# Kernel tuning notes

Hardware: AMD Instinct MI355X
Metric: run time of the kernel (lower is better)

Reference implementation:

```python
import jax, jax.numpy as jnp
import numpy as np

N_QUBITS = 10
N_LAYERS = 4
BATCH = 4096


def _apply_1q_batched(state, gate, q):
    # state: [B, 2,2,...,2]; gate: [B, 2, 2] (per-sample angles)
    s = jnp.moveaxis(state, 1 + q, -1)
    s = jnp.einsum('b...i,bji->b...j', s, gate)
    return jnp.moveaxis(s, -1, 1 + q)


def _apply_1q(state, gate, q):
    # gate: [2, 2] shared across batch
    s = jnp.moveaxis(state, 1 + q, -1)
    s = jnp.einsum('b...i,ji->b...j', s, gate)
    return jnp.moveaxis(s, -1, 1 + q)


def _apply_cnot(state, c, t):
    # bring control axis to 1 and target axis to 2, flip target where control==1
    s = jnp.moveaxis(state, (1 + c, 1 + t), (1, 2))
    s = jnp.concatenate([s[:, :1], s[:, 1:, ::-1]], axis=1)
    return jnp.moveaxis(s, (1, 2), (1 + c, 1 + t))


def _ry_rz_gate(theta_y, theta_z):
    # RZ(theta_z) @ RY(theta_y), both scalars -> [2, 2] complex
    hy = theta_y * 0.5
    cy, sy = jnp.cos(hy), jnp.sin(hy)
    ry = jnp.stack([jnp.stack([cy, -sy]), jnp.stack([sy, cy])]).astype(jnp.complex64)
    hz = theta_z * 0.5
    ph = jnp.exp(1j * jnp.stack([-hz, hz]).astype(jnp.complex64))  # diag of RZ
    return ph[:, None] * ry


def setup_inputs() -> dict:
    key = jax.random.key(0)
    kx, kp = jax.random.split(key)
    x = jax.random.uniform(kx, (BATCH, N_QUBITS), dtype=jnp.float32,
                           minval=-np.pi, maxval=np.pi)
    params = 0.5 * jax.random.normal(kp, (N_LAYERS, 2 * N_QUBITS), dtype=jnp.float32)
    return {"x": x, "params": params}


def reference(x, params):
    B, n = x.shape
    L = params.shape[0]
    dim = 2 ** n
    # |0...0> for every sample
    state = jnp.zeros((B, dim), jnp.complex64).at[:, 0].set(1.0)
    state = state.reshape((B,) + (2,) * n)

    # data encoding: RY(x[b, q]) on qubit q, per-sample angles
    half = x * 0.5
    c, s = jnp.cos(half), jnp.sin(half)  # [B, n]
    for q in range(n):
        g = jnp.stack([jnp.stack([c[:, q], -s[:, q]], -1),
                       jnp.stack([s[:, q], c[:, q]], -1)], -2).astype(jnp.complex64)  # [B,2,2]
        state = _apply_1q_batched(state, g, q)

    # variational layers: RY then RZ (fused) per qubit, then CNOT ring
    for l in range(L):
        for q in range(n):
            state = _apply_1q(state, _ry_rz_gate(params[l, q], params[l, n + q]), q)
        for q in range(n):
            state = _apply_cnot(state, q, (q + 1) % n)

    # <Z_q> = sum over basis states of |amp|^2 * (+1 if bit_q==0 else -1)
    probs = jnp.abs(state.reshape(B, dim)) ** 2  # float32 [B, 2^n]
    idx = jnp.arange(dim)
    bits = (idx[None, :] >> (n - 1 - jnp.arange(n))[:, None]) & 1  # [n, 2^n]
    signs = (1.0 - 2.0 * bits).astype(probs.dtype)
    return jnp.einsum('bs,qs->bq', probs, signs)  # [B, n]
```

## Files before the change

kernel.cpp:

```cpp
#include <hip/hip_runtime.h>

#define NQ 10

#if __has_builtin(__builtin_amdgcn_permlane16_swap)
#define HAVE_PLSWAP 1
#endif

typedef float v2f __attribute__((ext_vector_type(2)));

template<int M>
__device__ __forceinline__ float lx(float v) {
    if constexpr (M == 1)
        return __int_as_float(__builtin_amdgcn_mov_dpp(__float_as_int(v), 0xB1, 0xF, 0xF, true));
    else if constexpr (M == 2)
        return __int_as_float(__builtin_amdgcn_mov_dpp(__float_as_int(v), 0x4E, 0xF, 0xF, true));
    else if constexpr (M == 4) {
        int t = __builtin_amdgcn_mov_dpp(__float_as_int(v), 0x141, 0xF, 0xF, true);
        return __int_as_float(__builtin_amdgcn_mov_dpp(t, 0x1B, 0xF, 0xF, true));
    } else if constexpr (M == 8)
        return __int_as_float(__builtin_amdgcn_mov_dpp(__float_as_int(v), 0x128, 0xF, 0xF, true));
    else if constexpr (M == 16)
        return __int_as_float(__builtin_amdgcn_ds_swizzle(__float_as_int(v), (16 << 10) | 0x1F));
    else
        return __shfl_xor(v, M, 64);
}

template<int M>
__device__ __forceinline__ v2f lx2(v2f v) {
    v2f r;
    r.x = lx<M>(v.x);
    r.y = lx<M>(v.y);
    return r;
}

template<int M>
__device__ __forceinline__ void xch(float& a, float& b) {
#ifdef HAVE_PLSWAP
    if constexpr (M == 16) {
        auto r1 = __builtin_amdgcn_permlane16_swap(__float_as_uint(a), __float_as_uint(b), false, false);
        auto r2 = __builtin_amdgcn_permlane16_swap(r1[1], r1[0], false, false);
        a = __uint_as_float(r2[0]);
        b = __uint_as_float(r2[1]);
    } else {
        auto r1 = __builtin_amdgcn_permlane32_swap(__float_as_uint(a), __float_as_uint(b), false, false);
        auto r2 = __builtin_amdgcn_permlane32_swap(r1[1], r1[0], false, false);
        a = __uint_as_float(r2[0]);
        b = __uint_as_float(r2[1]);
    }
#else
    a = lx<M>(a);
    b = lx<M>(b);
#endif
}

template<int M>
__device__ __forceinline__ void xch2(v2f& a, v2f& b) {
    float ax = a.x, bx = b.x, ay = a.y, by = b.y;
    xch<M>(ax, bx);
    xch<M>(ay, by);
    a.x = ax; a.y = ay; b.x = bx; b.y = by;
}

__device__ __forceinline__ v2f cmul(v2f a, v2f b) {
    v2f n; n.x = -a.y; n.y = a.y;
    return a.xx * b + n * b.yx;
}

__device__ __forceinline__ v2f bperm2(int addr, v2f v) {
    v2f r;
    r.x = __int_as_float(__builtin_amdgcn_ds_bpermute(addr, __float_as_int(v.x)));
    r.y = __int_as_float(__builtin_amdgcn_ds_bpermute(addr, __float_as_int(v.y)));
    return r;
}

template<int M>
__device__ __forceinline__ void ry_lane(v2f st[16], int lane, float c, float s) {
    const float cB = (lane & M) ? s : -s;
#pragma unroll
    for (int r = 0; r < 16; ++r) {
        v2f part = lx2<M>(st[r]);
        st[r] = c * st[r] + cB * part;
    }
}

template<int M>
__device__ __forceinline__ void ry_lane_x(v2f st[16], int lane, float c, float s) {
    const float cB = (lane & M) ? s : -s;
#pragma unroll
    for (int r = 0; r < 16; r += 2) {
        v2f pa = st[r], pb = st[r + 1];
        xch2<M>(pa, pb);
        st[r]     = c * st[r]     + cB * pa;
        st[r + 1] = c * st[r + 1] + cB * pb;
    }
}

template<int RB>
__device__ __forceinline__ void ry_reg(v2f st[16], float c, float s) {
#pragma unroll
    for (int r = 0; r < 16; ++r) {
        if (r & RB) continue;
        v2f a0 = st[r], a1 = st[r | RB];
        st[r]      = c * a0 - s * a1;
        st[r | RB] = s * a0 + c * a1;
    }
}

template<int MC, int RB>
__device__ __forceinline__ void cnot_lane_reg(v2f st[16], int lane) {
    const bool sel = (lane & MC) != 0;
#pragma unroll
    for (int r = 0; r < 16; ++r) {
        if (r & RB) continue;
        v2f lo = st[r], hi = st[r | RB];
        st[r]      = sel ? hi : lo;
        st[r | RB] = sel ? lo : hi;
    }
}

template<int RC, int RT>
__device__ __forceinline__ void cnot_reg_reg(v2f st[16]) {
#pragma unroll
    for (int r = 0; r < 16; ++r) {
        if ((r & RC) && !(r & RT)) {
            v2f t = st[r];
            st[r] = st[r | RT];
            st[r | RT] = t;
        }
    }
}

__device__ __forceinline__ void cnot_q9_q0(v2f st[16]) {
#pragma unroll
    for (int i = 0; i < 4; ++i) {
        const int ra = 4 * i + 1, rb = 4 * i + 3;
        xch2<32>(st[ra], st[rb]);
    }
}

__device__ __forceinline__ float wht64(float v, int lane) {
    float t;
    t = lx<1>(v);  v = (lane & 1)  ? (t - v) : (v + t);
    t = lx<2>(v);  v = (lane & 2)  ? (t - v) : (v + t);
    t = lx<4>(v);  v = (lane & 4)  ? (t - v) : (v + t);
    t = lx<8>(v);  v = (lane & 8)  ? (t - v) : (v + t);
    t = lx<16>(v); v = (lane & 16) ? (t - v) : (v + t);
    t = lx<32>(v); v = (lane & 32) ? (t - v) : (v + t);
    return v;
}

__global__ __launch_bounds__(256)
void pqc_kernel(const float* __restrict__ x,
                const float* __restrict__ params,
                float* __restrict__ out, int B) {
    const int lane = threadIdx.x & 63;
    const int wave = threadIdx.x >> 6;
    const int b = blockIdx.x * 4 + wave;
    if (b >= B) return;

    const float* xb = x + (long)b * NQ;
    const float* p0 = params;
    float a0,b0,a1,b1,a2,b2,a3,b3,a4,b4,a5,b5,a6,b6,a7,b7,a8,b8,a9,b9;
    float cz0,sz0,cz1,sz1,cz2,sz2,cz3,sz3,cz4,sz4,cz5,sz5,cz6,sz6,cz7,sz7,cz8,sz8,cz9,sz9;
    __sincosf(0.5f * (xb[0] + p0[0]), &b0, &a0);
    __sincosf(0.5f * (xb[1] + p0[1]), &b1, &a1);
    __sincosf(0.5f * (xb[2] + p0[2]), &b2, &a2);
    __sincosf(0.5f * (xb[3] + p0[3]), &b3, &a3);
    __sincosf(0.5f * (xb[4] + p0[4]), &b4, &a4);
    __sincosf(0.5f * (xb[5] + p0[5]), &b5, &a5);
    __sincosf(0.5f * (xb[6] + p0[6]), &b6, &a6);
    __sincosf(0.5f * (xb[7] + p0[7]), &b7, &a7);
    __sincosf(0.5f * (xb[8] + p0[8]), &b8, &a8);
    __sincosf(0.5f * (xb[9] + p0[9]), &b9, &a9);
    __sincosf(0.5f * p0[10], &sz0, &cz0);
    __sincosf(0.5f * p0[11], &sz1, &cz1);
    __sincosf(0.5f * p0[12], &sz2, &cz2);
    __sincosf(0.5f * p0[13], &sz3, &cz3);
    __sincosf(0.5f * p0[14], &sz4, &cz4);
    __sincosf(0.5f * p0[15], &sz5, &cz5);
    __sincosf(0.5f * p0[16], &sz6, &cz6);
    __sincosf(0.5f * p0[17], &sz7, &cz7);
    __sincosf(0.5f * p0[18], &sz8, &cz8);
    __sincosf(0.5f * p0[19], &sz9, &cz9);

    float R = ((lane & 32) ? b0 : a0) * ((lane & 16) ? b1 : a1)
            * ((lane & 8)  ? b2 : a2) * ((lane & 4)  ? b3 : a3)
            * ((lane & 2)  ? b4 : a4) * ((lane & 1)  ? b5 : a5);
    v2f P; P.x = cz0; P.y = (lane & 32) ? sz0 : -sz0;
    { v2f t; t.x = cz1; t.y = (lane & 16) ? sz1 : -sz1; P = cmul(P, t); }
    { v2f t; t.x = cz2; t.y = (lane & 8)  ? sz2 : -sz2; P = cmul(P, t); }
    { v2f t; t.x = cz3; t.y = (lane & 4)  ? sz3 : -sz3; P = cmul(P, t); }
    { v2f t; t.x = cz4; t.y = (lane & 2)  ? sz4 : -sz4; P = cmul(P, t); }
    { v2f t; t.x = cz5; t.y = (lane & 1)  ? sz5 : -sz5; P = cmul(P, t); }
    v2f laneC = R * P;

    v2f u6l = { a6 * cz6, -a6 * sz6 }, u6h = { b6 * cz6, b6 * sz6 };
    v2f u7l = { a7 * cz7, -a7 * sz7 }, u7h = { b7 * cz7, b7 * sz7 };
    v2f u8l = { a8 * cz8, -a8 * sz8 }, u8h = { b8 * cz8, b8 * sz8 };
    v2f u9l = { a9 * cz9, -a9 * sz9 }, u9h = { b9 * cz9, b9 * sz9 };
    v2f A2[4] = { cmul(u6l, u7l), cmul(u6l, u7h), cmul(u6h, u7l), cmul(u6h, u7h) };
    v2f B2[4] = { cmul(u8l, u9l), cmul(u8l, u9h), cmul(u8h, u9l), cmul(u8h, u9h) };
    v2f LA[4] = { cmul(laneC, A2[0]), cmul(laneC, A2[1]),
                  cmul(laneC, A2[2]), cmul(laneC, A2[3]) };

    v2f st[16];
#pragma unroll
    for (int r = 0; r < 16; ++r) st[r] = cmul(LA[r >> 2], B2[r & 3]);

    {
        const int addr = ((lane ^ (lane >> 1)) & 63) << 2;
#pragma unroll
        for (int r = 0; r < 16; ++r) st[r] = bperm2(addr, st[r]);
        cnot_lane_reg<1, 8>(st, lane);
        cnot_reg_reg<8, 4>(st);
        cnot_reg_reg<4, 2>(st);
        cnot_reg_reg<2, 1>(st);
        cnot_q9_q0(st);
    }

    float c, s;
#pragma unroll
    for (int l = 1; l < 4; ++l) {
        const float* pl = params + l * 2 * NQ;

        __sincosf(0.5f * pl[0], &s, &c); ry_lane_x<32>(st, lane, c, s);
        __sincosf(0.5f * pl[1], &s, &c); ry_lane_x<16>(st, lane, c, s);
        __sincosf(0.5f * pl[2], &s, &c); ry_lane<8>(st, lane, c, s);
        __sincosf(0.5f * pl[3], &s, &c); ry_lane<4>(st, lane, c, s);
        __sincosf(0.5f * pl[4], &s, &c); ry_lane<2>(st, lane, c, s);
        __sincosf(0.5f * pl[5], &s, &c); ry_lane<1>(st, lane, c, s);
        __sincosf(0.5f * pl[6], &s, &c); ry_reg<8>(st, c, s);
        __sincosf(0.5f * pl[7], &s, &c); ry_reg<4>(st, c, s);
        __sincosf(0.5f * pl[8], &s, &c); ry_reg<2>(st, c, s);
        __sincosf(0.5f * pl[9], &s, &c); ry_reg<1>(st, c, s);

        if (l < 3) {
            float sz, cz;
            __sincosf(0.5f * pl[10], &sz, &cz);
            v2f PL; PL.x = cz; PL.y = (lane & 32) ? sz : -sz;
            __sincosf(0.5f * pl[11], &sz, &cz);
            { v2f t; t.x = cz; t.y = (lane & 16) ? sz : -sz; PL = cmul(PL, t); }
            __sincosf(0.5f * pl[12], &sz, &cz);
            { v2f t; t.x = cz; t.y = (lane & 8)  ? sz : -sz; PL = cmul(PL, t); }
            __sincosf(0.5f * pl[13], &sz, &cz);
            { v2f t; t.x = cz; t.y = (lane & 4)  ? sz : -sz; PL = cmul(PL, t); }
            __sincosf(0.5f * pl[14], &sz, &cz);
            { v2f t; t.x = cz; t.y = (lane & 2)  ? sz : -sz; PL = cmul(PL, t); }
            __sincosf(0.5f * pl[15], &sz, &cz);
            { v2f t; t.x = cz; t.y = (lane & 1)  ? sz : -sz; PL = cmul(PL, t); }

            float z6s, z6c, z7s, z7c, z8s, z8c, z9s, z9c;
            __sincosf(0.5f * pl[16], &z6s, &z6c);
            __sincosf(0.5f * pl[17], &z7s, &z7c);
            __sincosf(0.5f * pl[18], &z8s, &z8c);
            __sincosf(0.5f * pl[19], &z9s, &z9c);
            v2f A[4], Bb[4];
#pragma unroll
            for (int k = 0; k < 4; ++k) {
                v2f t6; t6.x = z6c; t6.y = (k & 2) ? z6s : -z6s;
                v2f t7; t7.x = z7c; t7.y = (k & 1) ? z7s : -z7s;
                A[k] = cmul(cmul(t6, t7), PL);
                v2f t8; t8.x = z8c; t8.y = (k & 2) ? z8s : -z8s;
                v2f t9; t9.x = z9c; t9.y = (k & 1) ? z9s : -z9s;
                Bb[k] = cmul(t8, t9);
            }
#pragma unroll
            for (int r = 0; r < 16; ++r)
                st[r] = cmul(cmul(st[r], A[r >> 2]), Bb[r & 3]);

            const int addr = ((lane ^ (lane >> 1)) & 63) << 2;
#pragma unroll
            for (int r = 0; r < 16; ++r) st[r] = bperm2(addr, st[r]);
            cnot_lane_reg<1, 8>(st, lane);
            cnot_reg_reg<8, 4>(st);
            cnot_reg_reg<4, 2>(st);
            cnot_reg_reg<2, 1>(st);
            cnot_q9_q0(st);
        }
    }

    float lane_sum = 0.f, A3 = 0.f, A32 = 0.f, A321 = 0.f, A3210 = 0.f;
#pragma unroll
    for (int r = 0; r < 16; ++r) {
        float p = st[r].x * st[r].x + st[r].y * st[r].y;
        const int p3 = (r >> 3) & 1;
        const int p32 = p3 ^ ((r >> 2) & 1);
        const int p321 = p32 ^ ((r >> 1) & 1);
        const int p3210 = p321 ^ (r & 1);
        lane_sum += p;
        A3    += p3    ? -p : p;
        A32   += p32   ? -p : p;
        A321  += p321  ? -p : p;
        A3210 += p3210 ? -p : p;
    }
    const float wLS   = wht64(lane_sum, lane);
    const float w3    = wht64(A3, lane);
    const float w32   = wht64(A32, lane);
    const float w321  = wht64(A321, lane);
    const float w3210 = wht64(A3210, lane);

    const long base = (long)b * NQ;
    if (lane == 31) out[base + 0] = w3210;
    if (lane == 48) out[base + 1] = wLS;
    if (lane == 56) out[base + 2] = wLS;
    if (lane == 60) out[base + 3] = wLS;
    if (lane == 62) out[base + 4] = wLS;
    if (lane == 63) {
        out[base + 5] = wLS;
        out[base + 6] = w3;
        out[base + 7] = w32;
        out[base + 8] = w321;
        out[base + 9] = w3210;
    }
}

extern "C" void kernel_launch(void* const* d_in, const int* in_sizes, int n_in,
                              void* d_out, int out_size, void* d_ws, size_t ws_size,
                              hipStream_t stream) {
    const float* x = (const float*)d_in[0];
    const float* params = (const float*)d_in[1];
    float* out = (float*)d_out;
    const int B = in_sizes[0] / NQ;
    const int grid = (B + 3) / 4;
    pqc_kernel<<<grid, 256, 0, stream>>>(x, params, out, B);
}
```

Before: 78.83 us.

## Absorb CNOT rings into GF(2) basis change instead of permuting amplitudes

```diff
diff --git a/kernel.cpp b/kernel.cpp
--- a/kernel.cpp
+++ b/kernel.cpp
@@ -2,63 +2,90 @@
 
 #define NQ 10
 
-#if __has_builtin(__builtin_amdgcn_permlane16_swap)
-#define HAVE_PLSWAP 1
-#endif
-
 typedef float v2f __attribute__((ext_vector_type(2)));
 
+struct M10 { unsigned r[10]; };
+
+constexpr M10 mk_R() {
+    M10 A{};
+    A.r[0] = 0b1111111110u;
+    for (int k = 1; k < 10; ++k) A.r[k] = (1u << (k + 1)) - 1u;
+    return A;
+}
+constexpr M10 mk_Rinv() {
+    M10 A{};
+    A.r[0] = (1u << 0) | (1u << 9);
+    A.r[1] = (1u << 0) | (1u << 1) | (1u << 9);
+    for (int k = 2; k < 10; ++k) A.r[k] = (1u << (k - 1)) | (1u << k);
+    return A;
+}
+constexpr M10 mmul(M10 A, M10 B) {
+    M10 C{};
+    for (int k = 0; k < 10; ++k) {
+        unsigned v = 0;
+        for (int j = 0; j < 10; ++j)
+            if ((A.r[k] >> j) & 1u) v ^= B.r[j];
+        C.r[k] = v;
+    }
+    return C;
+}
+constexpr M10 RF  = mk_R();
+constexpr M10 RV  = mk_Rinv();
+constexpr M10 RF2 = mmul(RF, RF);
+constexpr M10 RF3 = mmul(RF2, RF);
+constexpr M10 RF4 = mmul(RF2, RF2);
+constexpr M10 RV2 = mmul(RV, RV);
+constexpr M10 RV3 = mmul(RV2, RV);
+
+constexpr bool isI(M10 A) {
+    for (int k = 0; k < 10; ++k) if (A.r[k] != (1u << k)) return false;
+    return true;
+}
+static_assert(isI(mmul(RF, RV)), "Rinv wrong");
+static_assert(isI(mmul(RV3, RF3)), "powers wrong");
+
+constexpr unsigned colq(M10 A, int q) {
+    unsigned m = 0;
+    for (int k = 0; k < 10; ++k) m |= ((A.r[k] >> q) & 1u) << k;
+    return m;
+}
+constexpr int laneM(unsigned qm) {
+    int m = 0;
+    for (int q = 0; q <= 5; ++q) if ((qm >> q) & 1u) m |= 1 << (5 - q);
+    return m;
+}
+constexpr int regM(unsigned qm) {
+    int m = 0;
+    for (int q = 6; q <= 9; ++q) if ((qm >> q) & 1u) m |= 1 << (9 - q);
+    return m;
+}
+
+template<int CTRL>
+__device__ __forceinline__ float dppmov(float v) {
+    return __int_as_float(__builtin_amdgcn_mov_dpp(__float_as_int(v), CTRL, 0xF, 0xF, true));
+}
 template<int M>
 __device__ __forceinline__ float lx(float v) {
-    if constexpr (M == 1)
-        return __int_as_float(__builtin_amdgcn_mov_dpp(__float_as_int(v), 0xB1, 0xF, 0xF, true));
-    else if constexpr (M == 2)
-        return __int_as_float(__builtin_amdgcn_mov_dpp(__float_as_int(v), 0x4E, 0xF, 0xF, true));
-    else if constexpr (M == 4) {
-        int t = __builtin_amdgcn_mov_dpp(__float_as_int(v), 0x141, 0xF, 0xF, true);
-        return __int_as_float(__builtin_amdgcn_mov_dpp(t, 0x1B, 0xF, 0xF, true));
-    } else if constexpr (M == 8)
-        return __int_as_float(__builtin_amdgcn_mov_dpp(__float_as_int(v), 0x128, 0xF, 0xF, true));
-    else if constexpr (M == 16)
-        return __int_as_float(__builtin_amdgcn_ds_swizzle(__float_as_int(v), (16 << 10) | 0x1F));
+    static_assert(M > 0 && M < 64, "mask");
+    if constexpr (M == 1)       return dppmov<0xB1>(v);
+    else if constexpr (M == 2)  return dppmov<0x4E>(v);
+    else if constexpr (M == 3)  return dppmov<0x1B>(v);
+    else if constexpr (M == 7)  return dppmov<0x141>(v);
+    else if constexpr (M == 8)  return dppmov<0x128>(v);
+    else if constexpr (M == 15) return dppmov<0x140>(v);
+    else if constexpr (M == 4)  return lx<3>(lx<7>(v));
+    else if constexpr (M == 5)  return lx<2>(lx<7>(v));
+    else if constexpr (M == 6)  return lx<1>(lx<7>(v));
+    else if constexpr (M == 9)  return lx<1>(lx<8>(v));
+    else if constexpr (M == 10) return lx<2>(lx<8>(v));
+    else if constexpr (M == 11) return lx<3>(lx<8>(v));
+    else if constexpr (M == 12) return lx<3>(lx<15>(v));
+    else if constexpr (M == 13) return lx<2>(lx<15>(v));
+    else if constexpr (M == 14) return lx<1>(lx<15>(v));
+    else if constexpr (M < 32)
+        return __int_as_float(__builtin_amdgcn_ds_swizzle(__float_as_int(v), (M << 10) | 0x1F));
     else
         return __shfl_xor(v, M, 64);
-}
-
-template<int M>
-__device__ __forceinline__ v2f lx2(v2f v) {
-    v2f r;
-    r.x = lx<M>(v.x);
-    r.y = lx<M>(v.y);
-    return r;
-}
-
-template<int M>
-__device__ __forceinline__ void xch(float& a, float& b) {
-#ifdef HAVE_PLSWAP
-    if constexpr (M == 16) {
-        auto r1 = __builtin_amdgcn_permlane16_swap(__float_as_uint(a), __float_as_uint(b), false, false);
-        auto r2 = __builtin_amdgcn_permlane16_swap(r1[1], r1[0], false, false);
-        a = __uint_as_float(r2[0]);
-        b = __uint_as_float(r2[1]);
-    } else {
-        auto r1 = __builtin_amdgcn_permlane32_swap(__float_as_uint(a), __float_as_uint(b), false, false);
-        auto r2 = __builtin_amdgcn_permlane32_swap(r1[1], r1[0], false, false);
-        a = __uint_as_float(r2[0]);
-        b = __uint_as_float(r2[1]);
-    }
-#else
-    a = lx<M>(a);
-    b = lx<M>(b);
-#endif
-}
-
-template<int M>
-__device__ __forceinline__ void xch2(v2f& a, v2f& b) {
-    float ax = a.x, bx = b.x, ay = a.y, by = b.y;
-    xch<M>(ax, bx);
-    xch<M>(ay, by);
-    a.x = ax; a.y = ay; b.x = bx; b.y = by;
 }
 
 __device__ __forceinline__ v2f cmul(v2f a, v2f b) {
@@ -66,75 +93,70 @@
     return a.xx * b + n * b.yx;
 }
 
-__device__ __forceinline__ v2f bperm2(int addr, v2f v) {
-    v2f r;
-    r.x = __int_as_float(__builtin_amdgcn_ds_bpermute(addr, __float_as_int(v.x)));
-    r.y = __int_as_float(__builtin_amdgcn_ds_bpermute(addr, __float_as_int(v.y)));
-    return r;
-}
-
-template<int M>
-__device__ __forceinline__ void ry_lane(v2f st[16], int lane, float c, float s) {
-    const float cB = (lane & M) ? s : -s;
+template<int LM, int RM, int LW, int RW>
+__device__ __forceinline__ void ry_g(v2f st[16], int lane, float c, float s) {
+    static_assert((LM | RM) != 0, "null mask");
+    const float baseP = (__builtin_popcount((unsigned)(lane & LW)) & 1) ? s : -s;
+    if constexpr (RM == 0) {
+#pragma unroll
+        for (int r = 0; r < 16; ++r) {
+            v2f part;
+            part.x = lx<LM ? LM : 1>(st[r].x);
+            part.y = lx<LM ? LM : 1>(st[r].y);
+            const float cB = (__builtin_popcount((unsigned)(r & RW)) & 1) ? -baseP : baseP;
+            st[r] = c * st[r] + cB * part;
+        }
+    } else {
+        constexpr int PIV = RM & (-RM);
+#pragma unroll
+        for (int r = 0; r < 16; ++r) {
+            if (r & PIV) continue;
+            const int rb = r ^ RM;
+            v2f ea, eb;
+            if constexpr (LM != 0) {
+                ea.x = lx<LM ? LM : 1>(st[r].x);  ea.y = lx<LM ? LM : 1>(st[r].y);
+                eb.x = lx<LM ? LM : 1>(st[rb].x); eb.y = lx<LM ? LM : 1>(st[rb].y);
+            } else {
+                ea = st[r]; eb = st[rb];
+            }
+            const float cBa = (__builtin_popcount((unsigned)(r & RW)) & 1) ? -baseP : baseP;
+            const float cBb = (__builtin_popcount((unsigned)(rb & RW)) & 1) ? -baseP : baseP;
+            st[r]  = c * st[r]  + cBa * eb;
+            st[rb] = c * st[rb] + cBb * ea;
+        }
+    }
+}
+
+template<int L>
+__device__ __forceinline__ void diag_g(v2f st[16], int lane, const float* pl) {
+    constexpr M10 W = (L == 1) ? RF : RF2;
+    float G[16];
+#pragma unroll
+    for (int i = 0; i < 16; ++i) G[i] = 0.f;
+#pragma unroll
+    for (int q = 0; q < 10; ++q) {
+        const int LWq = laneM(W.r[q]);
+        const int RWq = regM(W.r[q]);
+        const float hz = 0.5f * pl[10 + q];
+        const float gq = (__builtin_popcount((unsigned)(lane & LWq)) & 1) ? hz : -hz;
+        G[RWq] += gq;
+    }
+#pragma unroll
+    for (int m = 1; m < 16; m <<= 1) {
+#pragma unroll
+        for (int r = 0; r < 16; ++r) {
+            if (r & m) continue;
+            const float a = G[r], bb = G[r | m];
+            G[r] = a + bb;
+            G[r | m] = a - bb;
+        }
+    }
 #pragma unroll
     for (int r = 0; r < 16; ++r) {
-        v2f part = lx2<M>(st[r]);
-        st[r] = c * st[r] + cB * part;
-    }
-}
-
-template<int M>
-__device__ __forceinline__ void ry_lane_x(v2f st[16], int lane, float c, float s) {
-    const float cB = (lane & M) ? s : -s;
-#pragma unroll
-    for (int r = 0; r < 16; r += 2) {
-        v2f pa = st[r], pb = st[r + 1];
-        xch2<M>(pa, pb);
-        st[r]     = c * st[r]     + cB * pa;
-        st[r + 1] = c * st[r + 1] + cB * pb;
-    }
-}
-
-template<int RB>
-__device__ __forceinline__ void ry_reg(v2f st[16], float c, float s) {
-#pragma unroll
-    for (int r = 0; r < 16; ++r) {
-        if (r & RB) continue;
-        v2f a0 = st[r], a1 = st[r | RB];
-        st[r]      = c * a0 - s * a1;
-        st[r | RB] = s * a0 + c * a1;
-    }
-}
-
-template<int MC, int RB>
-__device__ __forceinline__ void cnot_lane_reg(v2f st[16], int lane) {
-    const bool sel = (lane & MC) != 0;
-#pragma unroll
-    for (int r = 0; r < 16; ++r) {
-        if (r & RB) continue;
-        v2f lo = st[r], hi = st[r | RB];
-        st[r]      = sel ? hi : lo;
-        st[r | RB] = sel ? lo : hi;
-    }
-}
-
-template<int RC, int RT>
-__device__ __forceinline__ void cnot_reg_reg(v2f st[16]) {
-#pragma unroll
-    for (int r = 0; r < 16; ++r) {
-        if ((r & RC) && !(r & RT)) {
-            v2f t = st[r];
-            st[r] = st[r | RT];
-            st[r | RT] = t;
-        }
-    }
-}
-
-__device__ __forceinline__ void cnot_q9_q0(v2f st[16]) {
-#pragma unroll
-    for (int i = 0; i < 4; ++i) {
-        const int ra = 4 * i + 1, rb = 4 * i + 3;
-        xch2<32>(st[ra], st[rb]);
+        float sn, cs;
+        __sincosf(G[r], &sn, &cs);
+        v2f d; d.x = cs; d.y = sn;
+        st[r] = cmul(st[r], d);
     }
 }
 
@@ -207,110 +229,61 @@
 #pragma unroll
     for (int r = 0; r < 16; ++r) st[r] = cmul(LA[r >> 2], B2[r & 3]);
 
+#define GATE(INV, ROLE, Q, ANG) do { \
+    float gc_, gs_; __sincosf(0.5f * (ANG), &gs_, &gc_); \
+    ry_g<laneM(colq(INV, Q)), regM(colq(INV, Q)), \
+         laneM(ROLE.r[Q]), regM(ROLE.r[Q])>(st, lane, gc_, gs_); \
+} while (0)
+
     {
-        const int addr = ((lane ^ (lane >> 1)) & 63) << 2;
-#pragma unroll
-        for (int r = 0; r < 16; ++r) st[r] = bperm2(addr, st[r]);
-        cnot_lane_reg<1, 8>(st, lane);
-        cnot_reg_reg<8, 4>(st);
-        cnot_reg_reg<4, 2>(st);
-        cnot_reg_reg<2, 1>(st);
-        cnot_q9_q0(st);
-    }
-
-    float c, s;
-#pragma unroll
-    for (int l = 1; l < 4; ++l) {
-        const float* pl = params + l * 2 * NQ;
-
-        __sincosf(0.5f * pl[0], &s, &c); ry_lane_x<32>(st, lane, c, s);
-        __sincosf(0.5f * pl[1], &s, &c); ry_lane_x<16>(st, lane, c, s);
-        __sincosf(0.5f * pl[2], &s, &c); ry_lane<8>(st, lane, c, s);
-        __sincosf(0.5f * pl[3], &s, &c); ry_lane<4>(st, lane, c, s);
-        __sincosf(0.5f * pl[4], &s, &c); ry_lane<2>(st, lane, c, s);
-        __sincosf(0.5f * pl[5], &s, &c); ry_lane<1>(st, lane, c, s);
-        __sincosf(0.5f * pl[6], &s, &c); ry_reg<8>(st, c, s);
-        __sincosf(0.5f * pl[7], &s, &c); ry_reg<4>(st, c, s);
-        __sincosf(0.5f * pl[8], &s, &c); ry_reg<2>(st, c, s);
-        __sincosf(0.5f * pl[9], &s, &c); ry_reg<1>(st, c, s);
-
-        if (l < 3) {
-            float sz, cz;
-            __sincosf(0.5f * pl[10], &sz, &cz);
-            v2f PL; PL.x = cz; PL.y = (lane & 32) ? sz : -sz;
-            __sincosf(0.5f * pl[11], &sz, &cz);
-            { v2f t; t.x = cz; t.y = (lane & 16) ? sz : -sz; PL = cmul(PL, t); }
-            __sincosf(0.5f * pl[12], &sz, &cz);
-            { v2f t; t.x = cz; t.y = (lane & 8)  ? sz : -sz; PL = cmul(PL, t); }
-            __sincosf(0.5f * pl[13], &sz, &cz);
-            { v2f t; t.x = cz; t.y = (lane & 4)  ? sz : -sz; PL = cmul(PL, t); }
-            __sincosf(0.5f * pl[14], &sz, &cz);
-            { v2f t; t.x = cz; t.y = (lane & 2)  ? sz : -sz; PL = cmul(PL, t); }
-            __sincosf(0.5f * pl[15], &sz, &cz);
-            { v2f t; t.x = cz; t.y = (lane & 1)  ? sz : -sz; PL = cmul(PL, t); }
-
-            float z6s, z6c, z7s, z7c, z8s, z8c, z9s, z9c;
-            __sincosf(0.5f * pl[16], &z6s, &z6c);
-            __sincosf(0.5f * pl[17], &z7s, &z7c);
-            __sincosf(0.5f * pl[18], &z8s, &z8c);
-            __sincosf(0.5f * pl[19], &z9s, &z9c);
-            v2f A[4], Bb[4];
-#pragma unroll
-            for (int k = 0; k < 4; ++k) {
-                v2f t6; t6.x = z6c; t6.y = (k & 2) ? z6s : -z6s;
-                v2f t7; t7.x = z7c; t7.y = (k & 1) ? z7s : -z7s;
-                A[k] = cmul(cmul(t6, t7), PL);
-                v2f t8; t8.x = z8c; t8.y = (k & 2) ? z8s : -z8s;
-                v2f t9; t9.x = z9c; t9.y = (k & 1) ? z9s : -z9s;
-                Bb[k] = cmul(t8, t9);
-            }
-#pragma unroll
-            for (int r = 0; r < 16; ++r)
-                st[r] = cmul(cmul(st[r], A[r >> 2]), Bb[r & 3]);
-
-            const int addr = ((lane ^ (lane >> 1)) & 63) << 2;
-#pragma unroll
-            for (int r = 0; r < 16; ++r) st[r] = bperm2(addr, st[r]);
-            cnot_lane_reg<1, 8>(st, lane);
-            cnot_reg_reg<8, 4>(st);
-            cnot_reg_reg<4, 2>(st);
-            cnot_reg_reg<2, 1>(st);
-            cnot_q9_q0(st);
-        }
-    }
-
-    float lane_sum = 0.f, A3 = 0.f, A32 = 0.f, A321 = 0.f, A3210 = 0.f;
-#pragma unroll
-    for (int r = 0; r < 16; ++r) {
-        float p = st[r].x * st[r].x + st[r].y * st[r].y;
-        const int p3 = (r >> 3) & 1;
-        const int p32 = p3 ^ ((r >> 2) & 1);
-        const int p321 = p32 ^ ((r >> 1) & 1);
-        const int p3210 = p321 ^ (r & 1);
-        lane_sum += p;
-        A3    += p3    ? -p : p;
-        A32   += p32   ? -p : p;
-        A321  += p321  ? -p : p;
-        A3210 += p3210 ? -p : p;
-    }
-    const float wLS   = wht64(lane_sum, lane);
-    const float w3    = wht64(A3, lane);
-    const float w32   = wht64(A32, lane);
-    const float w321  = wht64(A321, lane);
-    const float w3210 = wht64(A3210, lane);
-
+        const float* pl = params + 20;
+        GATE(RV, RF, 0, pl[0]); GATE(RV, RF, 1, pl[1]);
+        GATE(RV, RF, 2, pl[2]); GATE(RV, RF, 3, pl[3]);
+        GATE(RV, RF, 4, pl[4]); GATE(RV, RF, 5, pl[5]);
+        GATE(RV, RF, 6, pl[6]); GATE(RV, RF, 7, pl[7]);
+        GATE(RV, RF, 8, pl[8]); GATE(RV, RF, 9, pl[9]);
+        diag_g<1>(st, lane, pl);
+    }
+    {
+        const float* pl = params + 40;
+        GATE(RV2, RF2, 0, pl[0]); GATE(RV2, RF2, 1, pl[1]);
+        GATE(RV2, RF2, 2, pl[2]); GATE(RV2, RF2, 3, pl[3]);
+        GATE(RV2, RF2, 4, pl[4]); GATE(RV2, RF2, 5, pl[5]);
+        GATE(RV2, RF2, 6, pl[6]); GATE(RV2, RF2, 7, pl[7]);
+        GATE(RV2, RF2, 8, pl[8]); GATE(RV2, RF2, 9, pl[9]);
+        diag_g<2>(st, lane, pl);
+    }
+    {
+        const float* pl = params + 60;
+        GATE(RV3, RF3, 0, pl[0]); GATE(RV3, RF3, 1, pl[1]);
+        GATE(RV3, RF3, 2, pl[2]); GATE(RV3, RF3, 3, pl[3]);
+        GATE(RV3, RF3, 4, pl[4]); GATE(RV3, RF3, 5, pl[5]);
+        GATE(RV3, RF3, 6, pl[6]); GATE(RV3, RF3, 7, pl[7]);
+        GATE(RV3, RF3, 8, pl[8]); GATE(RV3, RF3, 9, pl[9]);
+    }
+#undef GATE
+
+    float p[16];
+#pragma unroll
+    for (int r = 0; r < 16; ++r)
+        p[r] = st[r].x * st[r].x + st[r].y * st[r].y;
+#pragma unroll
+    for (int m = 1; m < 16; m <<= 1) {
+#pragma unroll
+        for (int r = 0; r < 16; ++r) {
+            if (r & m) continue;
+            const float a = p[r], bb = p[r | m];
+            p[r] = a + bb;
+            p[r | m] = a - bb;
+        }
+    }
     const long base = (long)b * NQ;
-    if (lane == 31) out[base + 0] = w3210;
-    if (lane == 48) out[base + 1] = wLS;
-    if (lane == 56) out[base + 2] = wLS;
-    if (lane == 60) out[base + 3] = wLS;
-    if (lane == 62) out[base + 4] = wLS;
-    if (lane == 63) {
-        out[base + 5] = wLS;
-        out[base + 6] = w3;
-        out[base + 7] = w32;
-        out[base + 8] = w321;
-        out[base + 9] = w3210;
+#pragma unroll
+    for (int q = 0; q < 10; ++q) {
+        const int LWq = laneM(RF4.r[q]);
+        const int RWq = regM(RF4.r[q]);
+        const float v = wht64(p[RWq], lane);
+        if (lane == LWq) out[base + q] = v;
     }
 }
 
```

Result: no change. 77.85 us (-1.2%).
